# Performance work log

Hardware: AMD Instinct MI355X
Metric: run time of the kernel (lower is better)

The kernel has to match this reference:

```python
import jax, jax.numpy as jnp
import numpy as np


def setup_inputs() -> dict:
    key = jax.random.key(0)
    ks = jax.random.split(key, 6)
    B, H, N, C, O, G = 4, 24, 512, 120, 512, 5
    x = jax.random.normal(ks[0], (B, H, N, C), dtype=jnp.float32)
    t_indices = jnp.arange(H, dtype=jnp.int64)
    time_emb = jax.random.normal(ks[1], (H, 8), dtype=jnp.float32)
    # kaiming-uniform-ish init for base linear weight
    fan_in = C + 8
    bound = float(np.sqrt(6.0 / fan_in))
    base_w = jax.random.uniform(ks[2], (O, C + 8), minval=-bound, maxval=bound, dtype=jnp.float32)
    base_b = jax.random.uniform(ks[3], (O,), minval=-1.0 / np.sqrt(fan_in), maxval=1.0 / np.sqrt(fan_in), dtype=jnp.float32)
    spline_weight = jax.random.uniform(ks[4], (O, C + 8, G), minval=-0.1, maxval=0.1, dtype=jnp.float32)
    return {"x": x, "t_indices": t_indices, "time_emb": time_emb,
            "base_w": base_w, "base_b": base_b, "spline_weight": spline_weight}


def reference(x, t_indices, time_emb, base_w, base_b, spline_weight):
    B, H, N, C = x.shape
    G = spline_weight.shape[-1]
    grid = jnp.linspace(-1.0, 1.0, G, dtype=x.dtype)  # non-trainable buffer
    # time embedding lookup, broadcast over batch and nodes: [B,H,N,8]
    t_emb = jnp.broadcast_to(time_emb[t_indices][None, :, None, :], (B, H, N, time_emb.shape[-1]))
    x_in = jnp.concatenate([x, t_emb], axis=-1)  # [B,H,N,C+8]
    # base path: SiLU then linear
    base = jnp.einsum('bhni,oi->bhno', jax.nn.silu(x_in), base_w) + base_b
    # RBF basis: [B,H,N,C+8,G]
    inv_h = (G - 1) / 2.0  # 1 / (2/(G-1))
    basis = jnp.exp(-(((x_in[..., None] - grid) * inv_h) ** 2))
    spline = jnp.einsum('bhnig,oig->bhno', basis, spline_weight)
    return base + spline
```

## Files before the change

kernel.cpp:

```cpp
#include <hip/hip_runtime.h>
#include <hip/hip_bf16.h>

typedef __attribute__((ext_vector_type(4))) float f32x4;
typedef __attribute__((ext_vector_type(8))) short bf16x8;

#define GLDS16(gp, lp) __builtin_amdgcn_global_load_lds( \
    (__attribute__((address_space(1))) void*)(void*)(gp), \
    (__attribute__((address_space(3))) void*)(lp), 16, 0, 0)

static constexpr int Mtot = 4 * 24 * 512;
static constexpr int Ktot = 128 * 6;
static constexpr int Otot = 512;
static constexpr int Hh   = 24;

__device__ inline unsigned short f2bf(float f) {
    __hip_bfloat16 h = __float2bfloat16(f);
    unsigned short u;
    __builtin_memcpy(&u, &h, 2);
    return u;
}

__device__ inline void feat6(float v, unsigned* o) {
    float f0 = v / (1.0f + __expf(-v));
    float r[5];
    #pragma unroll
    for (int g = 0; g < 5; ++g) {
        float t2 = 2.0f * (v - (-1.0f + 0.5f * g));
        r[g] = __expf(-t2 * t2);
    }
    o[0] = f2bf(f0)   | ((unsigned)f2bf(r[0]) << 16);
    o[1] = f2bf(r[1]) | ((unsigned)f2bf(r[2]) << 16);
    o[2] = f2bf(r[3]) | ((unsigned)f2bf(r[4]) << 16);
}

__global__ __launch_bounds__(256) void prep_A(
        const float* __restrict__ x, const int* __restrict__ t_idx,
        const float* __restrict__ temb, uint4* __restrict__ A4)
{
    int tid = blockIdx.x * 256 + threadIdx.x;
    int j = tid & 31;
    int m = tid >> 5;
    int h = (m >> 9) % Hh;
    float4 v4;
    if (j < 30) v4 = *(const float4*)(x + m * 120 + j * 4);
    else        v4 = *(const float4*)(temb + t_idx[h] * 8 + (j - 30) * 4);
    unsigned o[12];
    feat6(v4.x, o + 0);
    feat6(v4.y, o + 3);
    feat6(v4.z, o + 6);
    feat6(v4.w, o + 9);
    uint4* dst = A4 + tid * 3;
    dst[0] = make_uint4(o[0], o[1], o[2], o[3]);
    dst[1] = make_uint4(o[4], o[5], o[6], o[7]);
    dst[2] = make_uint4(o[8], o[9], o[10], o[11]);
}

__global__ __launch_bounds__(256) void prep_W(
        const float* __restrict__ bw, const float* __restrict__ sw,
        unsigned int* __restrict__ Wt)
{
    int tid = blockIdx.x * 256 + threadIdx.x;
    float f[6];
    f[0] = bw[tid];
    #pragma unroll
    for (int g = 0; g < 5; ++g) f[1 + g] = sw[tid * 5 + g];
    Wt[tid * 3 + 0] = f2bf(f[0]) | ((unsigned)f2bf(f[1]) << 16);
    Wt[tid * 3 + 1] = f2bf(f[2]) | ((unsigned)f2bf(f[3]) << 16);
    Wt[tid * 3 + 2] = f2bf(f[4]) | ((unsigned)f2bf(f[5]) << 16);
}

__global__ __launch_bounds__(256, 2) void gemm_kan(
        const __hip_bfloat16* __restrict__ A,
        const __hip_bfloat16* __restrict__ W,
        const float* __restrict__ bias,
        float* __restrict__ out)
{
    __shared__ char AsB[128 * 128];
    __shared__ char BsB[256 * 128];
    const int t    = threadIdx.x;
    const int wave = t >> 6;
    const int lane = t & 63;
    const int m_base = blockIdx.x * 128;
    const int n_base = blockIdx.y * 256;
    const int wm = (wave >> 1) * 64;
    const int wn = (wave & 1) * 128;
    const int ll = lane & 15;
    const int q4 = lane >> 4;

    f32x4 acc[4][8] = {};

    const int lr = t >> 3;
    const int s8 = t & 7;
    const int cg = s8 ^ (lr & 7);
    const __hip_bfloat16* ag = A + (long)(m_base + lr) * Ktot + cg * 8;
    const __hip_bfloat16* bg = W + (long)(n_base + lr) * Ktot + cg * 8;
    char* ldsA = AsB + wave * 1024;
    char* ldsB = BsB + wave * 1024;

    const int coff = ((q4 ^ (ll & 7)) * 16);
    const int aoff = (wm + ll) * 128 + coff;
    const int boff = (wn + ll) * 128 + coff;

    for (int kt = 0; kt < Ktot; kt += 64) {
        #pragma unroll
        for (int q = 0; q < 4; ++q)
            GLDS16(ag + kt + (long)q * 32 * Ktot, ldsA + q * 4096);
        #pragma unroll
        for (int q = 0; q < 8; ++q)
            GLDS16(bg + kt + (long)q * 32 * Ktot, ldsB + q * 4096);
        __syncthreads();
        #pragma unroll
        for (int kk = 0; kk < 2; ++kk) {
            const int ao = kk ? (aoff ^ 64) : aoff;
            const int bo = kk ? (boff ^ 64) : boff;
            bf16x8 af[4], bf[8];
            #pragma unroll
            for (int mi = 0; mi < 4; ++mi) af[mi] = *(const bf16x8*)(AsB + ao + mi * 2048);
            #pragma unroll
            for (int ni = 0; ni < 8; ++ni) bf[ni] = *(const bf16x8*)(BsB + bo + ni * 2048);
            #pragma unroll
            for (int mi = 0; mi < 4; ++mi)
                #pragma unroll
                for (int ni = 0; ni < 8; ++ni)
                    acc[mi][ni] = __builtin_amdgcn_mfma_f32_16x16x32_bf16(
                        af[mi], bf[ni], acc[mi][ni], 0, 0, 0);
        }
        __syncthreads();
    }

    const int col0 = n_base + wn + ll;
    const int row0 = m_base + wm + q4 * 4;
    #pragma unroll
    for (int ni = 0; ni < 8; ++ni) {
        const int col = col0 + ni * 16;
        const float bv = bias[col];
        #pragma unroll
        for (int mi = 0; mi < 4; ++mi) {
            #pragma unroll
            for (int r = 0; r < 4; ++r) {
                out[(long)(row0 + mi * 16 + r) * Otot + col] = acc[mi][ni][r] + bv;
            }
        }
    }
}

extern "C" void kernel_launch(void* const* d_in, const int* in_sizes, int n_in,
                              void* d_out, int out_size, void* d_ws, size_t ws_size,
                              hipStream_t stream) {
    const float* x    = (const float*)d_in[0];
    const int*   tidx = (const int*)  d_in[1];
    const float* temb = (const float*)d_in[2];
    const float* bw   = (const float*)d_in[3];
    const float* bb   = (const float*)d_in[4];
    const float* sw   = (const float*)d_in[5];
    float* out = (float*)d_out;

    __hip_bfloat16* A  = (__hip_bfloat16*)d_ws;
    __hip_bfloat16* Wt = (__hip_bfloat16*)((char*)d_ws + (size_t)Mtot * Ktot * 2);

    prep_A<<<Mtot * 32 / 256, 256, 0, stream>>>(x, tidx, temb, (uint4*)A);
    prep_W<<<Otot * 128 / 256, 256, 0, stream>>>(bw, sw, (unsigned int*)Wt);
    gemm_kan<<<dim3(Mtot / 128, Otot / 256), 256, 0, stream>>>(A, Wt, bb, out);
}
```

Baseline: 197.7 us.

## Fuse SiLU/RBF feature generation into GEMM A-tile loading, reorder K by feature

Drops the prep_A kernel and the 75 MB bf16 A matrix. The GEMM now reads fp32 x and the time embedding directly, computes SiLU or one RBF basis per K block, and writes the bf16 A tile to LDS. The weight layout is permuted so K is ordered feature-major (6 features × 128 inputs), which lets each K tile use a single basis function. The cost is recomputed transcendentals and repeated x reads for each of the 6 features and each N block, done synchronously with no overlap against the B loads.

```diff
diff --git a/kernel.cpp b/kernel.cpp
--- a/kernel.cpp
+++ b/kernel.cpp
@@ -9,7 +9,7 @@
     (__attribute__((address_space(3))) void*)(lp), 16, 0, 0)
 
 static constexpr int Mtot = 4 * 24 * 512;
-static constexpr int Ktot = 128 * 6;
+static constexpr int Ktot = 768;
 static constexpr int Otot = 512;
 static constexpr int Hh   = 24;
 
@@ -20,57 +20,32 @@
     return u;
 }
 
-__device__ inline void feat6(float v, unsigned* o) {
-    float f0 = v / (1.0f + __expf(-v));
-    float r[5];
-    #pragma unroll
-    for (int g = 0; g < 5; ++g) {
-        float t2 = 2.0f * (v - (-1.0f + 0.5f * g));
-        r[g] = __expf(-t2 * t2);
-    }
-    o[0] = f2bf(f0)   | ((unsigned)f2bf(r[0]) << 16);
-    o[1] = f2bf(r[1]) | ((unsigned)f2bf(r[2]) << 16);
-    o[2] = f2bf(r[3]) | ((unsigned)f2bf(r[4]) << 16);
-}
-
-__global__ __launch_bounds__(256) void prep_A(
-        const float* __restrict__ x, const int* __restrict__ t_idx,
-        const float* __restrict__ temb, uint4* __restrict__ A4)
+__global__ __launch_bounds__(256) void prep_W(
+        const float* __restrict__ bw, const float* __restrict__ sw,
+        uint2* __restrict__ Wt)
 {
     int tid = blockIdx.x * 256 + threadIdx.x;
-    int j = tid & 31;
-    int m = tid >> 5;
-    int h = (m >> 9) % Hh;
-    float4 v4;
-    if (j < 30) v4 = *(const float4*)(x + m * 120 + j * 4);
-    else        v4 = *(const float4*)(temb + t_idx[h] * 8 + (j - 30) * 4);
-    unsigned o[12];
-    feat6(v4.x, o + 0);
-    feat6(v4.y, o + 3);
-    feat6(v4.z, o + 6);
-    feat6(v4.w, o + 9);
-    uint4* dst = A4 + tid * 3;
-    dst[0] = make_uint4(o[0], o[1], o[2], o[3]);
-    dst[1] = make_uint4(o[4], o[5], o[6], o[7]);
-    dst[2] = make_uint4(o[8], o[9], o[10], o[11]);
-}
-
-__global__ __launch_bounds__(256) void prep_W(
-        const float* __restrict__ bw, const float* __restrict__ sw,
-        unsigned int* __restrict__ Wt)
-{
-    int tid = blockIdx.x * 256 + threadIdx.x;
-    float f[6];
-    f[0] = bw[tid];
-    #pragma unroll
-    for (int g = 0; g < 5; ++g) f[1 + g] = sw[tid * 5 + g];
-    Wt[tid * 3 + 0] = f2bf(f[0]) | ((unsigned)f2bf(f[1]) << 16);
-    Wt[tid * 3 + 1] = f2bf(f[2]) | ((unsigned)f2bf(f[3]) << 16);
-    Wt[tid * 3 + 2] = f2bf(f[4]) | ((unsigned)f2bf(f[5]) << 16);
+    int c4 = tid & 31;
+    int f  = (tid >> 5) % 6;
+    int o  = tid / 192;
+    int i  = c4 * 4;
+    float v[4];
+    if (f == 0) {
+        float4 t = *(const float4*)(bw + o * 128 + i);
+        v[0] = t.x; v[1] = t.y; v[2] = t.z; v[3] = t.w;
+    } else {
+        const float* sp = sw + (long)(o * 128 + i) * 5 + (f - 1);
+        v[0] = sp[0]; v[1] = sp[5]; v[2] = sp[10]; v[3] = sp[15];
+    }
+    uint2 w;
+    w.x = f2bf(v[0]) | ((unsigned)f2bf(v[1]) << 16);
+    w.y = f2bf(v[2]) | ((unsigned)f2bf(v[3]) << 16);
+    Wt[tid] = w;
 }
 
 __global__ __launch_bounds__(256, 2) void gemm_kan(
-        const __hip_bfloat16* __restrict__ A,
+        const float* __restrict__ x, const int* __restrict__ t_idx,
+        const float* __restrict__ temb,
         const __hip_bfloat16* __restrict__ W,
         const float* __restrict__ bias,
         float* __restrict__ out)
@@ -91,41 +66,78 @@
 
     const int lr = t >> 3;
     const int s8 = t & 7;
-    const int cg = s8 ^ (lr & 7);
-    const __hip_bfloat16* ag = A + (long)(m_base + lr) * Ktot + cg * 8;
-    const __hip_bfloat16* bg = W + (long)(n_base + lr) * Ktot + cg * 8;
-    char* ldsA = AsB + wave * 1024;
+    const int cgB = s8 ^ (lr & 7);
+    const __hip_bfloat16* bg = W + (long)(n_base + lr) * Ktot + cgB * 8;
     char* ldsB = BsB + wave * 1024;
 
-    const int coff = ((q4 ^ (ll & 7)) * 16);
+    const int c  = t & 15;
+    const int rb = t >> 4;
+
+    const int coff = (q4 ^ (ll & 7)) * 16;
     const int aoff = (wm + ll) * 128 + coff;
     const int boff = (wn + ll) * 128 + coff;
 
-    for (int kt = 0; kt < Ktot; kt += 64) {
+    for (int f6 = 0; f6 < 6; ++f6) {
+        const float gv = -1.0f + 0.5f * (float)(f6 - 1);
         #pragma unroll
-        for (int q = 0; q < 4; ++q)
-            GLDS16(ag + kt + (long)q * 32 * Ktot, ldsA + q * 4096);
-        #pragma unroll
-        for (int q = 0; q < 8; ++q)
-            GLDS16(bg + kt + (long)q * 32 * Ktot, ldsB + q * 4096);
-        __syncthreads();
-        #pragma unroll
-        for (int kk = 0; kk < 2; ++kk) {
-            const int ao = kk ? (aoff ^ 64) : aoff;
-            const int bo = kk ? (boff ^ 64) : boff;
-            bf16x8 af[4], bf[8];
+        for (int half = 0; half < 2; ++half) {
+            const int kt = (f6 * 2 + half) * 64;
             #pragma unroll
-            for (int mi = 0; mi < 4; ++mi) af[mi] = *(const bf16x8*)(AsB + ao + mi * 2048);
+            for (int q = 0; q < 8; ++q)
+                GLDS16(bg + kt + (long)q * 32 * Ktot, ldsB + q * 4096);
+
+            const int i = half * 64 + c * 4;
+            float4 xv[8];
             #pragma unroll
-            for (int ni = 0; ni < 8; ++ni) bf[ni] = *(const bf16x8*)(BsB + bo + ni * 2048);
+            for (int j = 0; j < 8; ++j) {
+                const int m = m_base + rb + j * 16;
+                if (i < 120) {
+                    xv[j] = *(const float4*)(x + (long)m * 120 + i);
+                } else {
+                    const int rt = t_idx[(m >> 9) % Hh];
+                    xv[j] = *(const float4*)(temb + rt * 8 + (i - 120));
+                }
+            }
             #pragma unroll
-            for (int mi = 0; mi < 4; ++mi)
+            for (int j = 0; j < 8; ++j) {
+                const int r = rb + j * 16;
+                float fv[4];
+                const float* vv = (const float*)&xv[j];
                 #pragma unroll
-                for (int ni = 0; ni < 8; ++ni)
-                    acc[mi][ni] = __builtin_amdgcn_mfma_f32_16x16x32_bf16(
-                        af[mi], bf[ni], acc[mi][ni], 0, 0, 0);
+                for (int e = 0; e < 4; ++e) {
+                    const float v = vv[e];
+                    if (f6 == 0) {
+                        fv[e] = v * __builtin_amdgcn_rcpf(1.0f + __expf(-v));
+                    } else {
+                        const float d = v - gv;
+                        fv[e] = __expf(-4.0f * d * d);
+                    }
+                }
+                uint2 w;
+                w.x = f2bf(fv[0]) | ((unsigned)f2bf(fv[1]) << 16);
+                w.y = f2bf(fv[2]) | ((unsigned)f2bf(fv[3]) << 16);
+                *(uint2*)(AsB + r * 128 + ((c >> 1) ^ (r & 7)) * 16 + (c & 1) * 8) = w;
+            }
+            __syncthreads();
+
+            #pragma unroll
+            for (int kk = 0; kk < 2; ++kk) {
+                const int ao = kk ? (aoff ^ 64) : aoff;
+                const int bo = kk ? (boff ^ 64) : boff;
+                bf16x8 af[4], bf[8];
+                #pragma unroll
+                for (int mi = 0; mi < 4; ++mi) af[mi] = *(const bf16x8*)(AsB + ao + mi * 2048);
+                #pragma unroll
+                for (int ni = 0; ni < 8; ++ni) bf[ni] = *(const bf16x8*)(BsB + bo + ni * 2048);
+                #pragma unroll
+                for (int mi = 0; mi < 4; ++mi)
+                    #pragma unroll
+                    for (int ni = 0; ni < 8; ++ni)
+                        acc[mi][ni] = __builtin_amdgcn_mfma_f32_16x16x32_bf16(
+                            af[mi], bf[ni], acc[mi][ni], 0, 0, 0);
+            }
+            __syncthreads();
         }
-        __syncthreads();
     }
 
     const int col0 = n_base + wn + ll;
@@ -155,10 +167,9 @@
     const float* sw   = (const float*)d_in[5];
     float* out = (float*)d_out;
 
-    __hip_bfloat16* A  = (__hip_bfloat16*)d_ws;
-    __hip_bfloat16* Wt = (__hip_bfloat16*)((char*)d_ws + (size_t)Mtot * Ktot * 2);
+    __hip_bfloat16* Wt = (__hip_bfloat16*)d_ws;
 
-    prep_A<<<Mtot * 32 / 256, 256, 0, stream>>>(x, tidx, temb, (uint4*)A);
-    prep_W<<<Otot * 128 / 256, 256, 0, stream>>>(bw, sw, (unsigned int*)Wt);
-    gemm_kan<<<dim3(Mtot / 128, Otot / 256), 256, 0, stream>>>(A, Wt, bb, out);
+    prep_W<<<Otot * 192 / 256, 256, 0, stream>>>(bw, sw, (uint2*)Wt);
+    gemm_kan<<<dim3(Mtot / 128, Otot / 256), 256, 0, stream>>>(
+        x, tidx, temb, Wt, bb, out);
 }
```

New measurement: 347.3 us. 1.76x slower.
